# Kernel optimization log

Measured on AMD Instinct MI355X. Metric: run time of the kernel, lower is better.

Reference implementation:

```python
import jax, jax.numpy as jnp
import numpy as np

B, S, D, H, BS, L, FF, V = 2, 4096, 1024, 16, 64, 4, 4096, 50000
HD = D // H; NB = S // BS; NM = NB - 2; R = 3

def layernorm(x, g, b):
    mu = x.mean(-1, keepdims=True)
    var = ((x - mu) ** 2).mean(-1, keepdims=True)
    return (x - mu) * jax.lax.rsqrt(var + 1e-5) * g + b

def bigbird_attn(x, neg, rand_attn, Wq, bq, Wk, bk, Wv, bv, Wo, bo):
    heads = lambda t: t.reshape(B, S, H, HD).transpose(0, 2, 1, 3)
    q, k, v = heads(x @ Wq + bq), heads(x @ Wk + bk), heads(x @ Wv + bv)
    scale = np.float32(1.0 / np.sqrt(HD))
    qb = q.reshape(B, H, NB, BS, HD); kb = k.reshape(B, H, NB, BS, HD); vb = v.reshape(B, H, NB, BS, HD)
    negb = neg.reshape(B, NB, BS)
    # global query blocks (first & last) attend densely to all keys
    qg = jnp.concatenate([qb[:, :, 0], qb[:, :, -1]], axis=2)  # [B,H,2*BS,HD]
    sg = jnp.einsum('bhqd,bhkd->bhqk', qg, k) * scale + neg[:, None, None, :]
    ctx_g = jnp.einsum('bhqk,bhkd->bhqd', jax.nn.softmax(sg, -1), v)
    # middle query blocks: sliding window(3) + global(2) + random(R) key blocks
    win_k = jnp.stack([kb[:, :, i:i + NM] for i in range(3)], axis=3)  # [B,H,NM,3,BS,HD]
    win_v = jnp.stack([vb[:, :, i:i + NM] for i in range(3)], axis=3)
    gidx = jnp.array([0, NB - 1])
    g_k = jnp.broadcast_to(kb[:, :, gidx][:, :, None], (B, H, NM, 2, BS, HD))
    g_v = jnp.broadcast_to(vb[:, :, gidx][:, :, None], (B, H, NM, 2, BS, HD))
    hix = jnp.arange(H)[:, None, None]
    r_k = kb[:, hix, rand_attn]  # [B,H,NM,R,BS,HD]
    r_v = vb[:, hix, rand_attn]
    K = 3 + 2 + R
    keys = jnp.concatenate([win_k, g_k, r_k], axis=3).reshape(B, H, NM, K * BS, HD)
    vals = jnp.concatenate([win_v, g_v, r_v], axis=3).reshape(B, H, NM, K * BS, HD)
    win_m = jnp.stack([negb[:, i:i + NM] for i in range(3)], axis=2)  # [B,NM,3,BS]
    g_m = jnp.broadcast_to(negb[:, gidx][:, None], (B, NM, 2, BS))
    m_wg = jnp.concatenate([win_m, g_m], axis=2).reshape(B, 1, NM, 5 * BS)
    r_m = negb[:, rand_attn].reshape(B, H, NM, R * BS)
    m_all = jnp.concatenate([jnp.broadcast_to(m_wg, (B, H, NM, 5 * BS)), r_m], axis=-1)
    sm = jnp.einsum('bhnqd,bhnkd->bhnqk', qb[:, :, 1:-1], keys) * scale + m_all[:, :, :, None, :]
    ctx_m = jnp.einsum('bhnqk,bhnkd->bhnqd', jax.nn.softmax(sm, -1), vals)
    ctx = jnp.concatenate([ctx_g[:, :, None, :BS], ctx_m, ctx_g[:, :, None, BS:]], axis=2)
    out = ctx.reshape(B, H, S, HD).transpose(0, 2, 1, 3).reshape(B, S, D)
    return out @ Wo + bo

def reference(input_ids, attention_mask, rand_attn, emb, Wq, bq, Wk, bk, Wv, bv, Wo, bo, ln1_g, ln1_b, W1, b1, W2, b2, ln2_g, ln2_b, lnf_g, lnf_b, projW, projb):
    x = emb[input_ids]
    neg = (1.0 - attention_mask.astype(jnp.float32)) * (-1e9)
    for l in range(L):  # pre-norm transformer encoder layers
        x = x + bigbird_attn(layernorm(x, ln1_g[l], ln1_b[l]), neg, rand_attn,
                             Wq[l], bq[l], Wk[l], bk[l], Wv[l], bv[l], Wo[l], bo[l])
        h = layernorm(x, ln2_g[l], ln2_b[l])
        x = x + (jax.nn.gelu(h @ W1[l] + b1[l]) @ W2[l] + b2[l])
    x = layernorm(x, lnf_g, lnf_b)
    feats = x.mean(axis=1)  # pooled output (mean over tokens)
    feats = feats / jnp.maximum(jnp.linalg.norm(feats, axis=-1, keepdims=True), 1e-12)
    return feats @ projW + projb

def setup_inputs():
    key = jax.random.key(0)
    ks = jax.random.split(key, 16)
    init = lambda k, shp: (0.02 * jax.random.normal(k, shp)).astype(jnp.float32)
    return {
        'input_ids': jax.random.randint(ks[0], (B, S), 0, V),
        'attention_mask': jnp.ones((B, S), dtype=jnp.int32),
        'rand_attn': jax.random.randint(ks[1], (H, NM, R), 1, NB - 1),
        'emb': init(ks[2], (V, D)),
        'Wq': init(ks[3], (L, D, D)), 'bq': jnp.zeros((L, D), jnp.float32),
        'Wk': init(ks[4], (L, D, D)), 'bk': jnp.zeros((L, D), jnp.float32),
        'Wv': init(ks[5], (L, D, D)), 'bv': jnp.zeros((L, D), jnp.float32),
        'Wo': init(ks[6], (L, D, D)), 'bo': jnp.zeros((L, D), jnp.float32),
        'ln1_g': jnp.ones((L, D), jnp.float32), 'ln1_b': jnp.zeros((L, D), jnp.float32),
        'W1': init(ks[7], (L, D, FF)), 'b1': jnp.zeros((L, FF), jnp.float32),
        'W2': init(ks[8], (L, FF, D)), 'b2': jnp.zeros((L, D), jnp.float32),
        'ln2_g': jnp.ones((L, D), jnp.float32), 'ln2_b': jnp.zeros((L, D), jnp.float32),
        'lnf_g': jnp.ones((D,), jnp.float32), 'lnf_b': jnp.zeros((D,), jnp.float32),
        'projW': init(ks[9], (D, 512)), 'projb': jnp.zeros((512,), jnp.float32),
    }
```

## Files before the change

### kernel.cpp

```cpp
#include <hip/hip_runtime.h>
#include <hip/hip_bf16.h>
#include <cstdint>
#include <cstddef>

#define BATCH 2
#define SEQ   4096
#define DIM   1024
#define NHEAD 16
#define HDIM  64
#define NBLK  64
#define NMID  62
#define NRAND 3
#define NLAYER 4
#define FFDIM 4096
#define ROWS  (BATCH*SEQ)
#define KSPL  8
#define QKVLD (3*DIM)

using f32x4 = __attribute__((ext_vector_type(4))) float;
using s16x8 = __attribute__((ext_vector_type(8))) short;
using s16x4 = __attribute__((ext_vector_type(4))) short;

__device__ inline float bf2f(short s) {
    unsigned u = ((unsigned)(unsigned short)s) << 16;
    union { unsigned u; float f; } cv; cv.u = u; return cv.f;
}
__device__ inline short f2bf(float f) {
    union { float f; unsigned u; } cv; cv.f = f;
    unsigned u = cv.u;
    unsigned r = (u + 0x7fffu + ((u >> 16) & 1u)) >> 16;
    return (short)r;
}
__device__ inline float gelu_f(float x) {
    float u = 0.7978845608028654f * (x + 0.044715f * x * x * x);
    float a = fabsf(u);
    float th = 1.f - 2.f / (1.f + __expf(2.f * a));
    th = copysignf(th, u);
    return 0.5f * x * (1.f + th);
}

__device__ inline void gload16(const short* g, short* l) {
    __builtin_amdgcn_global_load_lds(
        (const __attribute__((address_space(1))) void*)g,
        (__attribute__((address_space(3))) void*)l,
        16, 0, 0);
}

__global__ __launch_bounds__(256) void embed_kernel(
    const int* __restrict__ ids, const float* __restrict__ emb, float* __restrict__ x)
{
    int row = blockIdx.x;
    int id  = ids[row];
    ((float4*)x)[(size_t)row * 256 + threadIdx.x] =
        ((const float4*)emb)[(size_t)id * 256 + threadIdx.x];
}

__global__ __launch_bounds__(256) void neg_kernel(
    const int* __restrict__ mask, float* __restrict__ neg)
{
    int i = blockIdx.x * 256 + threadIdx.x;
    if (i < ROWS) neg[i] = (1.f - (float)mask[i]) * -1e9f;
}

__global__ __launch_bounds__(256) void biaspack_kernel(
    const float* __restrict__ bq, const float* __restrict__ bk,
    const float* __restrict__ bv, float* __restrict__ b3)
{
    int i = blockIdx.x * 256 + threadIdx.x;
    float v = (i < DIM) ? bq[i] : (i < 2 * DIM) ? bk[i - DIM] : bv[i - 2 * DIM];
    b3[i] = v;
}

template<int OUTBF>
__global__ __launch_bounds__(256) void ln_kernel(
    const float* __restrict__ x, const float* __restrict__ g,
    const float* __restrict__ bia, void* __restrict__ out)
{
    __shared__ float s1[4], s2[4];
    int row = blockIdx.x, t = threadIdx.x;
    const float* xr = x + (size_t)row * DIM;
    float4 v = ((const float4*)xr)[t];
    float s = v.x + v.y + v.z + v.w;
    #pragma unroll
    for (int o = 32; o > 0; o >>= 1) s += __shfl_xor(s, o, 64);
    if ((t & 63) == 0) s1[t >> 6] = s;
    __syncthreads();
    float mu = (s1[0] + s1[1] + s1[2] + s1[3]) * (1.f / DIM);
    float dx = v.x - mu, dy = v.y - mu, dz = v.z - mu, dw = v.w - mu;
    float q = dx*dx + dy*dy + dz*dz + dw*dw;
    #pragma unroll
    for (int o = 32; o > 0; o >>= 1) q += __shfl_xor(q, o, 64);
    if ((t & 63) == 0) s2[t >> 6] = q;
    __syncthreads();
    float var = (s2[0] + s2[1] + s2[2] + s2[3]) * (1.f / DIM);
    float rs  = rsqrtf(var + 1e-5f);
    float4 gg = ((const float4*)g)[t];
    float4 bb = ((const float4*)bia)[t];
    float o0 = dx * rs * gg.x + bb.x;
    float o1 = dy * rs * gg.y + bb.y;
    float o2 = dz * rs * gg.z + bb.z;
    float o3 = dw * rs * gg.w + bb.w;
    if (OUTBF) {
        s16x4 ov = { f2bf(o0), f2bf(o1), f2bf(o2), f2bf(o3) };
        ((s16x4*)out)[(size_t)row * (DIM/4) + t] = ov;
    } else {
        float4 ov = { o0, o1, o2, o3 };
        ((float4*)out)[(size_t)row * (DIM/4) + t] = ov;
    }
}

__global__ __launch_bounds__(256) void wconv_kernel(
    const float* __restrict__ W, short* __restrict__ Wt, int K, int N)
{
    __shared__ float tile[32][33];
    int k0 = blockIdx.x * 32, n0 = blockIdx.y * 32;
    int t = threadIdx.x;
    int r = t >> 3, c = (t & 7) * 4;
    float4 v = *(const float4*)(W + (size_t)(k0 + r) * N + n0 + c);
    tile[r][c+0] = v.x; tile[r][c+1] = v.y; tile[r][c+2] = v.z; tile[r][c+3] = v.w;
    __syncthreads();
    s16x4 ov;
    #pragma unroll
    for (int jj = 0; jj < 4; ++jj) ov[jj] = f2bf(tile[c + jj][r]);
    *(s16x4*)(Wt + (size_t)(n0 + r) * K + k0 + c) = ov;
}

__global__ __launch_bounds__(256) void vtrans_kernel(
    const short* __restrict__ qkv, short* __restrict__ vT)
{
    __shared__ short tile[64][66];
    const int sb = blockIdx.x, h = blockIdx.y, b = blockIdx.z;
    const int t = threadIdx.x;
    {
        int row = t >> 2, c0 = (t & 3) * 16;
        const short* src = qkv + 2 * DIM + (size_t)(b * SEQ + sb * 64 + row) * QKVLD + h * HDIM + c0;
        s16x8 a0 = ((const s16x8*)src)[0];
        s16x8 a1 = ((const s16x8*)src)[1];
        #pragma unroll
        for (int i = 0; i < 8; ++i) { tile[row][c0 + i] = a0[i]; tile[row][c0 + 8 + i] = a1[i]; }
    }
    __syncthreads();
    {
        int d = t >> 2, k0 = (t & 3) * 16;
        s16x8 o0, o1;
        #pragma unroll
        for (int i = 0; i < 8; ++i) { o0[i] = tile[k0 + i][d]; o1[i] = tile[k0 + 8 + i][d]; }
        short* dst = vT + (size_t)((b * NHEAD + h) * HDIM + d) * SEQ + sb * 64 + k0;
        ((s16x8*)dst)[0] = o0;
        ((s16x8*)dst)[1] = o1;
    }
}

template<int EPI>
__global__ __launch_bounds__(512) void gemm256_kernel(
    const short* __restrict__ A, const short* __restrict__ Bt,
    const float* __restrict__ bias, const float* __restrict__ resid,
    void* __restrict__ Cout, int M, int N, int K, int klen)
{
    __shared__ short As[2][256 * 64];
    __shared__ short Bs[2][256 * 64];
    const int t = threadIdx.x;
    const int m0 = blockIdx.x * 256, n0 = blockIdx.y * 256;
    const int lane = t & 63, wave = t >> 6;
    const int wm = wave >> 2, wn = wave & 3;
    const int lrow = lane >> 3;
    const int lksw = ((lane & 7) ^ lrow) * 8;

    f32x4 acc[8][4];
    #pragma unroll
    for (int m = 0; m < 8; ++m)
        #pragma unroll
        for (int n = 0; n < 4; ++n)
            acc[m][n] = f32x4{0.f, 0.f, 0.f, 0.f};

    auto STAGE = [&](int side, int kt) {
        #pragma unroll
        for (int c = 0; c < 4; ++c) {
            int chunk = wave + c * 8;
            int row = chunk * 8 + lrow;
            gload16(A  + (size_t)(m0 + row) * K + kt + lksw, &As[side][chunk * 512]);
            gload16(Bt + (size_t)(n0 + row) * K + kt + lksw, &Bs[side][chunk * 512]);
        }
    };

    const int k0 = blockIdx.z * klen;
    STAGE(0, k0);
    __syncthreads();

    int cur = 0;
    for (int kt = k0; kt < k0 + klen; kt += 64) {
        if (kt + 64 < k0 + klen) STAGE(cur ^ 1, kt + 64);
        const short* Ac = As[cur];
        const short* Bc = Bs[cur];
        #pragma unroll
        for (int kk = 0; kk < 2; ++kk) {
            const int cb = kk * 64 + (lane >> 4) * 16;
            s16x8 bfr[4];
            #pragma unroll
            for (int n = 0; n < 4; ++n) {
                int rB = wn * 64 + n * 16 + (lane & 15);
                bfr[n] = *(const s16x8*)((const char*)Bc + rB * 128 + (cb ^ ((rB & 7) << 4)));
            }
            #pragma unroll
            for (int mq = 0; mq < 4; ++mq) {
                s16x8 af[2];
                #pragma unroll
                for (int i = 0; i < 2; ++i) {
                    int rA = wm * 128 + mq * 32 + i * 16 + (lane & 15);
                    af[i] = *(const s16x8*)((const char*)Ac + rA * 128 + (cb ^ ((rA & 7) << 4)));
                }
                #pragma unroll
                for (int i = 0; i < 2; ++i)
                    #pragma unroll
                    for (int n = 0; n < 4; ++n)
                        acc[mq * 2 + i][n] = __builtin_amdgcn_mfma_f32_16x16x32_bf16(
                            af[i], bfr[n], acc[mq * 2 + i][n], 0, 0, 0);
            }
        }
        __syncthreads();
        cur ^= 1;
    }

    const int rbase = m0 + wm * 128 + ((lane >> 4) << 2);
    const int cbase = n0 + wn * 64 + (lane & 15);
    #pragma unroll
    for (int m = 0; m < 8; ++m) {
        #pragma unroll
        for (int n = 0; n < 4; ++n) {
            #pragma unroll
            for (int j = 0; j < 4; ++j) {
                int row = rbase + m * 16 + j;
                int col = cbase + n * 16;
                size_t idx = (size_t)row * N + col;
                float val = acc[m][n][j];
                if (EPI == 3) {
                    ((float*)Cout)[(size_t)blockIdx.z * ((size_t)M * N) + idx] = val;
                } else {
                    val += bias[col];
                    if (EPI == 1) val = gelu_f(val);
                    ((short*)Cout)[idx] = f2bf(val);
                }
            }
        }
    }
    (void)resid;
}

template<int EPI>
__global__ __launch_bounds__(256) void gemm_kernel(
    const short* __restrict__ A, const short* __restrict__ Bt,
    const float* __restrict__ bias, const float* __restrict__ resid,
    void* __restrict__ Cout, int M, int N, int K, int klen)
{
    __shared__ short As[128 * 64];
    __shared__ short Bs[128 * 64];
    const int t = threadIdx.x;
    const int m0 = blockIdx.x * 128, n0 = blockIdx.y * 128;
    const int lane = t & 63, wave = t >> 6;
    const int wr = (wave >> 1) * 64, wc = (wave & 1) * 64;
    const int lrow = lane >> 3;
    const int lksw = ((lane & 7) ^ lrow) * 8;

    f32x4 acc[4][4];
    #pragma unroll
    for (int m = 0; m < 4; ++m)
        #pragma unroll
        for (int n = 0; n < 4; ++n)
            acc[m][n] = f32x4{0.f, 0.f, 0.f, 0.f};

    const int k0 = blockIdx.z * klen;
    for (int kt = k0; kt < k0 + klen; kt += 64) {
        #pragma unroll
        for (int c = 0; c < 4; ++c) {
            int chunk = wave * 4 + c;
            int row = chunk * 8 + lrow;
            gload16(A  + (size_t)(m0 + row) * K + kt + lksw, As + chunk * 512);
            gload16(Bt + (size_t)(n0 + row) * K + kt + lksw, Bs + chunk * 512);
        }
        asm volatile("s_waitcnt vmcnt(0)" ::: "memory");
        __syncthreads();
        #pragma unroll
        for (int kk = 0; kk < 2; ++kk) {
            s16x8 af[4], bfr[4];
            int cb = kk * 64 + (lane >> 4) * 16;
            #pragma unroll
            for (int i = 0; i < 4; ++i) {
                int rA = wr + i * 16 + (lane & 15);
                af[i]  = *(const s16x8*)((const char*)As + rA * 128 + (cb ^ ((rA & 7) << 4)));
                int rB = wc + i * 16 + (lane & 15);
                bfr[i] = *(const s16x8*)((const char*)Bs + rB * 128 + (cb ^ ((rB & 7) << 4)));
            }
            #pragma unroll
            for (int m = 0; m < 4; ++m)
                #pragma unroll
                for (int n = 0; n < 4; ++n)
                    acc[m][n] = __builtin_amdgcn_mfma_f32_16x16x32_bf16(
                        af[m], bfr[n], acc[m][n], 0, 0, 0);
        }
        __syncthreads();
    }

    const int rbase = m0 + wr + ((lane >> 4) << 2);
    const int cbase = n0 + wc + (lane & 15);
    #pragma unroll
    for (int m = 0; m < 4; ++m) {
        #pragma unroll
        for (int n = 0; n < 4; ++n) {
            #pragma unroll
            for (int j = 0; j < 4; ++j) {
                int row = rbase + m * 16 + j;
                int col = cbase + n * 16;
                size_t idx = (size_t)row * N + col;
                float val = acc[m][n][j] + bias[col];
                if (EPI == 1) val = gelu_f(val);
                if (EPI == 2) ((float*)Cout)[idx] = val + resid[idx];
                else          ((short*)Cout)[idx] = f2bf(val);
            }
        }
    }
}

__global__ __launch_bounds__(256) void kred_kernel(
    const float* __restrict__ part, const float* __restrict__ bias, float* __restrict__ x)
{
    const size_t MN = (size_t)ROWS * DIM;
    size_t idx = (size_t)blockIdx.x * DIM + threadIdx.x * 4;
    float4 p0 = *(const float4*)(part + idx);
    float4 p1 = *(const float4*)(part + MN + idx);
    float4 bb = *(const float4*)(bias + threadIdx.x * 4);
    float4 xv = *(const float4*)(x + idx);
    float4 o = { xv.x + p0.x + p1.x + bb.x,
                 xv.y + p0.y + p1.y + bb.y,
                 xv.z + p0.z + p1.z + bb.z,
                 xv.w + p0.w + p1.w + bb.w };
    *(float4*)(x + idx) = o;
}

__device__ inline void attn_tile_mfma(
    const short* __restrict__ kglob, const short* __restrict__ vtglob,
    const float* __restrict__ negp, int kld,
    short* Ks, short* Vs, float* kmask,
    const s16x8* qfrag, f32x4* o, float& mr, float& lsum)
{
    const int t = threadIdx.x;
    const int lane = t & 63;
    const int q15 = lane & 15, g = lane >> 4;
    const int sw = (lane & 7) << 4;

    {
        int row = t >> 2, c0 = (t & 3) * 16;
        int rsw = (row & 7) << 4;
        const short* ksrc = kglob + (size_t)row * kld + c0;
        s16x8 a0 = ((const s16x8*)ksrc)[0];
        s16x8 a1 = ((const s16x8*)ksrc)[1];
        char* kdst = (char*)Ks + row * 128;
        *(s16x8*)(kdst + ((c0 * 2)      ^ rsw)) = a0;
        *(s16x8*)(kdst + ((c0 * 2 + 16) ^ rsw)) = a1;
        const short* vsrc = vtglob + (size_t)row * SEQ + c0;
        s16x8 b0 = ((const s16x8*)vsrc)[0];
        s16x8 b1 = ((const s16x8*)vsrc)[1];
        char* vdst = (char*)Vs + row * 128;
        *(s16x8*)(vdst + ((c0 * 2)      ^ rsw)) = b0;
        *(s16x8*)(vdst + ((c0 * 2 + 16) ^ rsw)) = b1;
        if (t < 16) ((float4*)kmask)[t] = ((const float4*)negp)[t];
    }
    __syncthreads();

    f32x4 s[4];
    #pragma unroll
    for (int f = 0; f < 4; ++f) s[f] = f32x4{0.f, 0.f, 0.f, 0.f};
    #pragma unroll
    for (int ch = 0; ch < 2; ++ch) {
        #pragma unroll
        for (int f = 0; f < 4; ++f) {
            s16x8 kf = *(const s16x8*)((const char*)Ks + (16 * f + q15) * 128 + ((ch * 64 + g * 16) ^ sw));
            s[f] = __builtin_amdgcn_mfma_f32_16x16x32_bf16(kf, qfrag[ch], s[f], 0, 0, 0);
        }
    }

    float p[4][4];
    float mt = -1e30f;
    #pragma unroll
    for (int f = 0; f < 4; ++f) {
        float4 km = ((const float4*)kmask)[f * 4 + g];
        #pragma unroll
        for (int j = 0; j < 4; ++j) {
            float val = s[f][j] * 0.125f + ((const float*)&km)[j];
            p[f][j] = val;
            mt = fmaxf(mt, val);
        }
    }
    mt = fmaxf(mt, __shfl_xor(mt, 16, 64));
    mt = fmaxf(mt, __shfl_xor(mt, 32, 64));
    float mn = fmaxf(mr, mt);
    float psum = 0.f;
    #pragma unroll
    for (int f = 0; f < 4; ++f)
        #pragma unroll
        for (int j = 0; j < 4; ++j) {
            float e = __expf(p[f][j] - mn);
            p[f][j] = e;
            psum += e;
        }
    psum += __shfl_xor(psum, 16, 64);
    psum += __shfl_xor(psum, 32, 64);
    float fc = __expf(mr - mn);
    mr = mn;
    lsum = lsum * fc + psum;
    #pragma unroll
    for (int dt = 0; dt < 4; ++dt)
        #pragma unroll
        for (int j = 0; j < 4; ++j) o[dt][j] *= fc;

    unsigned pk[4][2];
    #pragma unroll
    for (int f = 0; f < 4; ++f)
        #pragma unroll
        for (int pp = 0; pp < 2; ++pp)
            pk[f][pp] = ((unsigned)(unsigned short)f2bf(p[f][2 * pp + 1]) << 16)
                      |  (unsigned)(unsigned short)f2bf(p[f][2 * pp]);

    const int bsel = (lane >> 4) & 1, asel = (lane >> 5) & 1;
    #pragma unroll
    for (int c = 0; c < 2; ++c) {
        union { s16x8 v; int u[4]; } pb;
        #pragma unroll
        for (int w = 0; w < 4; ++w) {
            int src = q15 + 16 * (2 * bsel + (w >> 1));
            int lo = __shfl((int)pk[2 * c][w & 1], src, 64);
            int hi = __shfl((int)pk[2 * c + 1][w & 1], src, 64);
            pb.u[w] = asel ? hi : lo;
        }
        #pragma unroll
        for (int dt = 0; dt < 4; ++dt) {
            s16x8 vf = *(const s16x8*)((const char*)Vs + (16 * dt + q15) * 128 + ((c * 64 + g * 16) ^ sw));
            o[dt] = __builtin_amdgcn_mfma_f32_16x16x32_bf16(vf, pb.v, o[dt], 0, 0, 0);
        }
    }
    __syncthreads();
}

__device__ inline void stage_q64_swz(const short* __restrict__ qglob, int qld, short* Qs)
{
    int t = threadIdx.x;
    int row = t >> 2, c0 = (t & 3) * 16;
    int rsw = (row & 7) << 4;
    const short* src = qglob + (size_t)row * qld + c0;
    s16x8 a0 = ((const s16x8*)src)[0];
    s16x8 a1 = ((const s16x8*)src)[1];
    char* dst = (char*)Qs + row * 128;
    *(s16x8*)(dst + ((c0 * 2)      ^ rsw)) = a0;
    *(s16x8*)(dst + ((c0 * 2 + 16) ^ rsw)) = a1;
}

__global__ __launch_bounds__(256) void attn_middle_mfma(
    const short* __restrict__ qkv, const short* __restrict__ vT,
    const float* __restrict__ neg, const int* __restrict__ rand_attn, short* __restrict__ ctx)
{
    __shared__ short Qs[64 * 64];
    __shared__ short Ks[64 * 64];
    __shared__ short Vs[64 * 64];
    __shared__ float kmask[64];

    const int j = blockIdx.x, h = blockIdx.y, b = blockIdx.z;
    const int n = j + 1;
    const int t = threadIdx.x;
    const int lane = t & 63, wave = t >> 6;
    const int q15 = lane & 15, g = lane >> 4;
    const int sw = (lane & 7) << 4;

    stage_q64_swz(qkv + (size_t)(b * SEQ + n * 64) * QKVLD + h * HDIM, QKVLD, Qs);
    __syncthreads();

    s16x8 qfrag[2];
    {
        int qrow = wave * 16 + q15;
        #pragma unroll
        for (int ch = 0; ch < 2; ++ch)
            qfrag[ch] = *(const s16x8*)((const char*)Qs + qrow * 128 + ((ch * 64 + g * 16) ^ sw));
    }

    int kbl[8];
    kbl[0] = n - 1; kbl[1] = n; kbl[2] = n + 1; kbl[3] = 0; kbl[4] = NBLK - 1;
    {
        const int* ra = rand_attn + ((size_t)h * NMID + j) * NRAND;
        kbl[5] = ra[0]; kbl[6] = ra[1]; kbl[7] = ra[2];
    }

    f32x4 o[4];
    #pragma unroll
    for (int dt = 0; dt < 4; ++dt) o[dt] = f32x4{0.f, 0.f, 0.f, 0.f};
    float mr = -1e30f, lsum = 0.f;

    const short* kbase  = qkv + DIM + (size_t)b * SEQ * QKVLD + h * HDIM;
    const short* vtbase = vT + (size_t)(b * NHEAD + h) * HDIM * SEQ;
    const float* negb   = neg + (size_t)b * SEQ;

    #pragma unroll 1
    for (int ib = 0; ib < 8; ++ib) {
        int kbn = kbl[ib];
        attn_tile_mfma(kbase + (size_t)kbn * 64 * QKVLD, vtbase + kbn * 64,
                       negb + kbn * 64, QKVLD, Ks, Vs, kmask, qfrag, o, mr, lsum);
    }

    float inv = 1.f / lsum;
    short* obase = ctx + (size_t)(b * SEQ + n * 64 + wave * 16 + q15) * DIM + h * HDIM;
    #pragma unroll
    for (int dt = 0; dt < 4; ++dt) {
        s16x4 ov;
        #pragma unroll
        for (int jj = 0; jj < 4; ++jj) ov[jj] = f2bf(o[dt][jj] * inv);
        *(s16x4*)(obase + dt * 16 + g * 4) = ov;
    }
}

__global__ __launch_bounds__(256) void attn_global_mfma(
    const short* __restrict__ qkv, const short* __restrict__ vT,
    const float* __restrict__ neg, float* __restrict__ part)
{
    __shared__ short Qs[64 * 64];
    __shared__ short Ks[64 * 64];
    __shared__ short Vs[64 * 64];
    __shared__ float kmask[64];

    const int qb = blockIdx.x >> 3, ks = blockIdx.x & 7;
    const int h = blockIdx.y, b = blockIdx.z;
    const int tok0 = qb ? (SEQ - 64) : 0;
    const int t = threadIdx.x;
    const int lane = t & 63, wave = t >> 6;
    const int q15 = lane & 15, g = lane >> 4;
    const int sw = (lane & 7) << 4;

    stage_q64_swz(qkv + (size_t)(b * SEQ + tok0) * QKVLD + h * HDIM, QKVLD, Qs);
    __syncthreads();

    s16x8 qfrag[2];
    {
        int qrow = wave * 16 + q15;
        #pragma unroll
        for (int ch = 0; ch < 2; ++ch)
            qfrag[ch] = *(const s16x8*)((const char*)Qs + qrow * 128 + ((ch * 64 + g * 16) ^ sw));
    }

    f32x4 o[4];
    #pragma unroll
    for (int dt = 0; dt < 4; ++dt) o[dt] = f32x4{0.f, 0.f, 0.f, 0.f};
    float mr = -1e30f, lsum = 0.f;

    const short* kbase  = qkv + DIM + (size_t)b * SEQ * QKVLD + h * HDIM;
    const short* vtbase = vT + (size_t)(b * NHEAD + h) * HDIM * SEQ;
    const float* negb   = neg + (size_t)b * SEQ;

    #pragma unroll 1
    for (int ib = 0; ib < 8; ++ib) {
        int kbn = ks * 8 + ib;
        attn_tile_mfma(kbase + (size_t)kbn * 64 * QKVLD, vtbase + kbn * 64,
                       negb + kbn * 64, QKVLD, Ks, Vs, kmask, qfrag, o, mr, lsum);
    }

    float* pbase = part + ((size_t)(((b * NHEAD + h) * 2 + qb) * KSPL + ks)) * 4224;
    int qrow = wave * 16 + q15;
    #pragma unroll
    for (int dt = 0; dt < 4; ++dt)
        *(f32x4*)(pbase + qrow * 64 + dt * 16 + g * 4) = o[dt];
    if (g == 0) { pbase[4096 + qrow] = mr; pbase[4160 + qrow] = lsum; }
}

__global__ __launch_bounds__(256) void attn_greduce(
    const float* __restrict__ part, short* __restrict__ ctx)
{
    const int qb = blockIdx.x, h = blockIdx.y, b = blockIdx.z;
    const int tok0 = qb ? (SEQ - 64) : 0;
    const int t = threadIdx.x;
    const int qq = t >> 2, d0 = (t & 3) * 16;
    const float* base = part + ((size_t)(((b * NHEAD + h) * 2 + qb) * KSPL)) * 4224;

    float m = -1e30f;
    #pragma unroll 1
    for (int s = 0; s < KSPL; ++s)
        m = fmaxf(m, base[(size_t)s * 4224 + 4096 + qq]);
    float L = 0.f;
    float acc[16];
    #pragma unroll
    for (int i = 0; i < 16; ++i) acc[i] = 0.f;
    #pragma unroll 1
    for (int s = 0; s < KSPL; ++s) {
        const float* bp = base + (size_t)s * 4224;
        float w = __expf(bp[4096 + qq] - m);
        L += w * bp[4160 + qq];
        const float4* row = (const float4*)(bp + qq * 64 + d0);
        #pragma unroll
        for (int v4 = 0; v4 < 4; ++v4) {
            float4 val = row[v4];
            acc[v4 * 4 + 0] = fmaf(w, val.x, acc[v4 * 4 + 0]);
            acc[v4 * 4 + 1] = fmaf(w, val.y, acc[v4 * 4 + 1]);
            acc[v4 * 4 + 2] = fmaf(w, val.z, acc[v4 * 4 + 2]);
            acc[v4 * 4 + 3] = fmaf(w, val.w, acc[v4 * 4 + 3]);
        }
    }
    float inv = 1.f / L;
    short* dst = ctx + (size_t)(b * SEQ + tok0 + qq) * DIM + h * HDIM + d0;
    s16x8 o0, o1;
    #pragma unroll
    for (int i = 0; i < 8; ++i) { o0[i] = f2bf(acc[i] * inv); o1[i] = f2bf(acc[8 + i] * inv); }
    ((s16x8*)dst)[0] = o0;
    ((s16x8*)dst)[1] = o1;
}

__global__ __launch_bounds__(256) void colsum1_kernel(
    const float* __restrict__ xln, float* __restrict__ partial)
{
    const int ch = blockIdx.x, b = blockIdx.y, t = threadIdx.x;
    const float* base = xln + ((size_t)b * SEQ + ch * 32) * DIM + t * 4;
    float4 acc = {0.f, 0.f, 0.f, 0.f};
    #pragma unroll 4
    for (int r = 0; r < 32; ++r) {
        float4 v = *(const float4*)(base + (size_t)r * DIM);
        acc.x += v.x; acc.y += v.y; acc.z += v.z; acc.w += v.w;
    }
    *(float4*)(partial + ((size_t)(b * 128 + ch)) * DIM + t * 4) = acc;
}

__global__ __launch_bounds__(256) void colsum2_kernel(
    const float* __restrict__ partial, float* __restrict__ feats)
{
    const int b = blockIdx.x, t = threadIdx.x;
    float4 acc = {0.f, 0.f, 0.f, 0.f};
    #pragma unroll 1
    for (int ch = 0; ch < 128; ++ch) {
        float4 v = *(const float4*)(partial + ((size_t)(b * 128 + ch)) * DIM + t * 4);
        acc.x += v.x; acc.y += v.y; acc.z += v.z; acc.w += v.w;
    }
    const float is = 1.f / SEQ;
    float4 o = { acc.x * is, acc.y * is, acc.z * is, acc.w * is };
    *(float4*)(feats + (size_t)b * DIM + t * 4) = o;
}

__global__ __launch_bounds__(256) void head_kernel(
    const float* __restrict__ feats, const float* __restrict__ projW,
    const float* __restrict__ projb, float* __restrict__ out)
{
    __shared__ float f[DIM];
    __shared__ float slots[4];
    int b = blockIdx.x, t = threadIdx.x;
    float ss = 0.f;
    for (int i = t; i < DIM; i += 256) {
        float vv = feats[b * DIM + i];
        f[i] = vv;
        ss += vv * vv;
    }
    #pragma unroll
    for (int o = 32; o > 0; o >>= 1) ss += __shfl_xor(ss, o, 64);
    if ((t & 63) == 0) slots[t >> 6] = ss;
    __syncthreads();
    float nrm = sqrtf(slots[0] + slots[1] + slots[2] + slots[3]);
    float inv = 1.f / fmaxf(nrm, 1e-12f);
    for (int o = t; o < 512; o += 256) {
        float acc = 0.f;
        for (int d = 0; d < DIM; ++d)
            acc = fmaf(f[d], projW[(size_t)d * 512 + o], acc);
        out[b * 512 + o] = acc * inv + projb[o];
    }
}

extern "C" void kernel_launch(void* const* d_in, const int* in_sizes, int n_in,
                              void* d_out, int out_size, void* d_ws, size_t ws_size,
                              hipStream_t stream)
{
    (void)in_sizes; (void)n_in; (void)out_size; (void)ws_size;
    const int*   ids   = (const int*)d_in[0];
    const int*   amask = (const int*)d_in[1];
    const int*   rnd   = (const int*)d_in[2];
    const float* emb   = (const float*)d_in[3];
    const float* Wq    = (const float*)d_in[4];
    const float* bq    = (const float*)d_in[5];
    const float* Wk    = (const float*)d_in[6];
    const float* bk    = (const float*)d_in[7];
    const float* Wv    = (const float*)d_in[8];
    const float* bv    = (const float*)d_in[9];
    const float* Wo    = (const float*)d_in[10];
    const float* bo    = (const float*)d_in[11];
    const float* ln1g  = (const float*)d_in[12];
    const float* ln1b  = (const float*)d_in[13];
    const float* W1    = (const float*)d_in[14];
    const float* b1    = (const float*)d_in[15];
    const float* W2    = (const float*)d_in[16];
    const float* b2    = (const float*)d_in[17];
    const float* ln2g  = (const float*)d_in[18];
    const float* ln2b  = (const float*)d_in[19];
    const float* lnfg  = (const float*)d_in[20];
    const float* lnfb  = (const float*)d_in[21];
    const float* projW = (const float*)d_in[22];
    const float* projb = (const float*)d_in[23];
    float* out = (float*)d_out;

    char* ws = (char*)d_ws;
    size_t off = 0;
    float* x    = (float*)(ws + off); off += (size_t)ROWS * DIM * 4;
    float* xn_f = (float*)(ws + off);
    short* xn_b = (short*)(ws + off); off += (size_t)ROWS * DIM * 4;
    short* qkv  = (short*)(ws + off); off += (size_t)ROWS * QKVLD * 2;
    short* vT   = (short*)(ws + off); off += (size_t)ROWS * DIM * 2;
    short* ctxb = (short*)(ws + off); off += (size_t)ROWS * DIM * 2;
    short* ffb  = (short*)(ws + off); off += (size_t)ROWS * FFDIM * 2;
    short* wt   = (short*)(ws + off); off += (size_t)FFDIM * DIM * 2;
    float* neg  = (float*)(ws + off); off += (size_t)ROWS * 4;
    float* bias3= (float*)(ws + off); off += (size_t)QKVLD * 4;
    float* feats= (float*)(ws + off); off += (size_t)BATCH * DIM * 4;
    float* part = (float*)(ws + off); off += (size_t)BATCH * NHEAD * 2 * KSPL * 4224 * 4;
    float* cpart= (float*)(ws + off); off += (size_t)BATCH * 128 * DIM * 4;
    float* ff2p = (float*)qkv;

    embed_kernel<<<ROWS, 256, 0, stream>>>(ids, emb, x);
    neg_kernel<<<(ROWS + 255) / 256, 256, 0, stream>>>(amask, neg);

    for (int l = 0; l < NLAYER; ++l) {
        ln_kernel<1><<<ROWS, 256, 0, stream>>>(x, ln1g + l * DIM, ln1b + l * DIM, xn_b);

        wconv_kernel<<<dim3(DIM/32, DIM/32), 256, 0, stream>>>(Wq + (size_t)l*DIM*DIM, wt,               DIM, DIM);
        wconv_kernel<<<dim3(DIM/32, DIM/32), 256, 0, stream>>>(Wk + (size_t)l*DIM*DIM, wt + 1024*1024,   DIM, DIM);
        wconv_kernel<<<dim3(DIM/32, DIM/32), 256, 0, stream>>>(Wv + (size_t)l*DIM*DIM, wt + 2*1024*1024, DIM, DIM);
        biaspack_kernel<<<QKVLD/256, 256, 0, stream>>>(bq + l*DIM, bk + l*DIM, bv + l*DIM, bias3);
        gemm256_kernel<0><<<dim3(ROWS/256, QKVLD/256), 512, 0, stream>>>(xn_b, wt, bias3, nullptr, qkv, ROWS, QKVLD, DIM, DIM);

        vtrans_kernel<<<dim3(SEQ/64, NHEAD, BATCH), 256, 0, stream>>>(qkv, vT);

        attn_global_mfma<<<dim3(2 * KSPL, NHEAD, BATCH), 256, 0, stream>>>(qkv, vT, neg, part);
        attn_middle_mfma<<<dim3(NMID, NHEAD, BATCH), 256, 0, stream>>>(qkv, vT, neg, rnd, ctxb);
        attn_greduce<<<dim3(2, NHEAD, BATCH), 256, 0, stream>>>(part, ctxb);

        wconv_kernel<<<dim3(DIM/32, DIM/32), 256, 0, stream>>>(Wo + (size_t)l*DIM*DIM, wt, DIM, DIM);
        gemm_kernel<2><<<dim3(ROWS/128, DIM/128), 256, 0, stream>>>(ctxb, wt, bo + l*DIM, x, x, ROWS, DIM, DIM, DIM);

        ln_kernel<1><<<ROWS, 256, 0, stream>>>(x, ln2g + l * DIM, ln2b + l * DIM, xn_b);

        wconv_kernel<<<dim3(DIM/32, FFDIM/32), 256, 0, stream>>>(W1 + (size_t)l*DIM*FFDIM, wt, DIM, FFDIM);
        gemm256_kernel<1><<<dim3(ROWS/256, FFDIM/256), 512, 0, stream>>>(xn_b, wt, b1 + l*FFDIM, nullptr, ffb, ROWS, FFDIM, DIM, DIM);
        wconv_kernel<<<dim3(FFDIM/32, DIM/32), 256, 0, stream>>>(W2 + (size_t)l*FFDIM*DIM, wt, FFDIM, DIM);
        gemm256_kernel<3><<<dim3(ROWS/256, DIM/256, 2), 512, 0, stream>>>(ffb, wt, nullptr, nullptr, ff2p, ROWS, DIM, FFDIM, FFDIM/2);
        kred_kernel<<<ROWS, 256, 0, stream>>>(ff2p, b2 + l*DIM, x);
    }

    ln_kernel<0><<<ROWS, 256, 0, stream>>>(x, lnfg, lnfb, xn_f);
    colsum1_kernel<<<dim3(SEQ/32, BATCH), 256, 0, stream>>>(xn_f, cpart);
    colsum2_kernel<<<BATCH, 256, 0, stream>>>(cpart, feats);
    head_kernel<<<BATCH, 256, 0, stream>>>(feats, projW, projb, out);
}
```

Before: 1.774 ms.

## Batch weight conversion upfront, triple-buffer GEMM with 256x128 tiles, fuse residual-reduce with LayerNorm

All layers' weights are converted to transposed bf16 in a few batched launches before the layer loop, replacing the many per-layer small conversion kernels. The 256-wide GEMM now uses 256x128 tiles with three LDS stages, explicit vmcnt waits, raw barriers and setprio, to overlap global loads with MFMA work and add more workgroups. The split-K reduction kernel is fused with the following LayerNorm, which drops a separate LN pass over the activations per layer. The cost is a larger workspace holding all layers' converted weights, and hand-written waitcnt logic that depends on the exact count of loads issued per stage.

New measurement: 2.196 ms. 23.8% more time.

```diff
diff --git a/kernel.cpp b/kernel.cpp
--- a/kernel.cpp
+++ b/kernel.cpp
@@ -16,6 +16,7 @@
 #define ROWS  (BATCH*SEQ)
 #define KSPL  8
 #define QKVLD (3*DIM)
+#define WLAYER (12*1024*1024)
 
 using f32x4 = __attribute__((ext_vector_type(4))) float;
 using s16x8 = __attribute__((ext_vector_type(8))) short;
@@ -67,8 +68,11 @@
     const float* __restrict__ bv, float* __restrict__ b3)
 {
     int i = blockIdx.x * 256 + threadIdx.x;
-    float v = (i < DIM) ? bq[i] : (i < 2 * DIM) ? bk[i - DIM] : bv[i - 2 * DIM];
-    b3[i] = v;
+    int l = blockIdx.y;
+    float v = (i < DIM) ? bq[l * DIM + i]
+            : (i < 2 * DIM) ? bk[l * DIM + i - DIM]
+            : bv[l * DIM + i - 2 * DIM];
+    b3[(size_t)l * QKVLD + i] = v;
 }
 
 template<int OUTBF>
@@ -109,8 +113,8 @@
     }
 }
 
-__global__ __launch_bounds__(256) void wconv_kernel(
-    const float* __restrict__ W, short* __restrict__ Wt, int K, int N)
+__device__ inline void wconv_body(const float* __restrict__ W, short* __restrict__ Wt,
+                                  int K, int N)
 {
     __shared__ float tile[32][33];
     int k0 = blockIdx.x * 32, n0 = blockIdx.y * 32;
@@ -123,6 +127,25 @@
     #pragma unroll
     for (int jj = 0; jj < 4; ++jj) ov[jj] = f2bf(tile[c + jj][r]);
     *(s16x4*)(Wt + (size_t)(n0 + r) * K + k0 + c) = ov;
+}
+
+__global__ __launch_bounds__(256) void wconv4_kernel(
+    const float* __restrict__ Wq, const float* __restrict__ Wk,
+    const float* __restrict__ Wv, const float* __restrict__ Wo,
+    short* __restrict__ wt4)
+{
+    int z = blockIdx.z, l = z >> 2, m = z & 3;
+    const float* W = (m == 0 ? Wq : m == 1 ? Wk : m == 2 ? Wv : Wo) + (size_t)l * DIM * DIM;
+    short* Wt = wt4 + (size_t)l * WLAYER + (size_t)m * 1024 * 1024;
+    wconv_body(W, Wt, DIM, DIM);
+}
+
+__global__ __launch_bounds__(256) void wconvff_kernel(
+    const float* __restrict__ W, short* __restrict__ wt4,
+    int K, int N, size_t dstOff)
+{
+    int l = blockIdx.z;
+    wconv_body(W + (size_t)l * DIM * FFDIM, wt4 + (size_t)l * WLAYER + dstOff, K, N);
 }
 
 __global__ __launch_bounds__(256) void vtrans_kernel(
@@ -154,79 +177,100 @@
 template<int EPI>
 __global__ __launch_bounds__(512) void gemm256_kernel(
     const short* __restrict__ A, const short* __restrict__ Bt,
-    const float* __restrict__ bias, const float* __restrict__ resid,
-    void* __restrict__ Cout, int M, int N, int K, int klen)
-{
-    __shared__ short As[2][256 * 64];
-    __shared__ short Bs[2][256 * 64];
+    const float* __restrict__ bias, void* __restrict__ Cout,
+    int M, int N, int K, int klen)
+{
+    __shared__ short As[3][256 * 64];
+    __shared__ short Bs[3][128 * 64];
     const int t = threadIdx.x;
-    const int m0 = blockIdx.x * 256, n0 = blockIdx.y * 256;
+    const int m0 = blockIdx.x * 256, n0 = blockIdx.y * 128;
     const int lane = t & 63, wave = t >> 6;
     const int wm = wave >> 2, wn = wave & 3;
+    const int l15 = lane & 15;
     const int lrow = lane >> 3;
     const int lksw = ((lane & 7) ^ lrow) * 8;
 
-    f32x4 acc[8][4];
+    f32x4 acc[8][2];
     #pragma unroll
     for (int m = 0; m < 8; ++m)
         #pragma unroll
-        for (int n = 0; n < 4; ++n)
+        for (int n = 0; n < 2; ++n)
             acc[m][n] = f32x4{0.f, 0.f, 0.f, 0.f};
 
     auto STAGE = [&](int side, int kt) {
         #pragma unroll
         for (int c = 0; c < 4; ++c) {
-            int chunk = wave + c * 8;
-            int row = chunk * 8 + lrow;
-            gload16(A  + (size_t)(m0 + row) * K + kt + lksw, &As[side][chunk * 512]);
-            gload16(Bt + (size_t)(n0 + row) * K + kt + lksw, &Bs[side][chunk * 512]);
+            int chunk = wave * 4 + c;
+            gload16(A + (size_t)(m0 + chunk * 8 + lrow) * K + kt + lksw,
+                    &As[side][chunk * 512]);
+        }
+        #pragma unroll
+        for (int c = 0; c < 2; ++c) {
+            int chunk = wave * 2 + c;
+            gload16(Bt + (size_t)(n0 + chunk * 8 + lrow) * K + kt + lksw,
+                    &Bs[side][chunk * 512]);
         }
     };
 
     const int k0 = blockIdx.z * klen;
+    const int T = klen >> 6;
     STAGE(0, k0);
-    __syncthreads();
-
-    int cur = 0;
-    for (int kt = k0; kt < k0 + klen; kt += 64) {
-        if (kt + 64 < k0 + klen) STAGE(cur ^ 1, kt + 64);
-        const short* Ac = As[cur];
-        const short* Bc = Bs[cur];
-        #pragma unroll
-        for (int kk = 0; kk < 2; ++kk) {
-            const int cb = kk * 64 + (lane >> 4) * 16;
-            s16x8 bfr[4];
+    if (T > 1) {
+        STAGE(1, k0 + 64);
+        asm volatile("s_waitcnt vmcnt(6)" ::: "memory");
+    } else {
+        asm volatile("s_waitcnt vmcnt(0)" ::: "memory");
+    }
+    __builtin_amdgcn_s_barrier();
+
+    for (int ti = 0; ti < T; ++ti) {
+        const int side = ti % 3;
+        if (ti + 2 < T) STAGE((ti + 2) % 3, k0 + (ti + 2) * 64);
+
+        const short* Ac = As[side];
+        const short* Bc = Bs[side];
+        s16x8 bfr[2][2];
+        #pragma unroll
+        for (int nf = 0; nf < 2; ++nf)
             #pragma unroll
-            for (int n = 0; n < 4; ++n) {
-                int rB = wn * 64 + n * 16 + (lane & 15);
-                bfr[n] = *(const s16x8*)((const char*)Bc + rB * 128 + (cb ^ ((rB & 7) << 4)));
+            for (int kk = 0; kk < 2; ++kk) {
+                int r = wn * 32 + nf * 16 + l15;
+                int cb = kk * 64 + (lane >> 4) * 16;
+                bfr[nf][kk] = *(const s16x8*)((const char*)Bc + r * 128 + (cb ^ ((r & 7) << 4)));
+            }
+        __builtin_amdgcn_s_setprio(1);
+        #pragma unroll
+        for (int mf = 0; mf < 8; ++mf) {
+            s16x8 af[2];
+            #pragma unroll
+            for (int kk = 0; kk < 2; ++kk) {
+                int r = wm * 128 + mf * 16 + l15;
+                int cb = kk * 64 + (lane >> 4) * 16;
+                af[kk] = *(const s16x8*)((const char*)Ac + r * 128 + (cb ^ ((r & 7) << 4)));
             }
             #pragma unroll
-            for (int mq = 0; mq < 4; ++mq) {
-                s16x8 af[2];
+            for (int kk = 0; kk < 2; ++kk)
                 #pragma unroll
-                for (int i = 0; i < 2; ++i) {
-                    int rA = wm * 128 + mq * 32 + i * 16 + (lane & 15);
-                    af[i] = *(const s16x8*)((const char*)Ac + rA * 128 + (cb ^ ((rA & 7) << 4)));
-                }
-                #pragma unroll
-                for (int i = 0; i < 2; ++i)
-                    #pragma unroll
-                    for (int n = 0; n < 4; ++n)
-                        acc[mq * 2 + i][n] = __builtin_amdgcn_mfma_f32_16x16x32_bf16(
-                            af[i], bfr[n], acc[mq * 2 + i][n], 0, 0, 0);
-            }
-        }
-        __syncthreads();
-        cur ^= 1;
+                for (int nf = 0; nf < 2; ++nf)
+                    acc[mf][nf] = __builtin_amdgcn_mfma_f32_16x16x32_bf16(
+                        af[kk], bfr[nf][kk], acc[mf][nf], 0, 0, 0);
+        }
+        __builtin_amdgcn_s_setprio(0);
+        __builtin_amdgcn_sched_barrier(0);
+        if (ti + 2 < T) {
+            asm volatile("s_waitcnt vmcnt(6)" ::: "memory");
+        } else if (ti + 1 < T) {
+            asm volatile("s_waitcnt vmcnt(0)" ::: "memory");
+        }
+        __builtin_amdgcn_s_barrier();
     }
 
     const int rbase = m0 + wm * 128 + ((lane >> 4) << 2);
-    const int cbase = n0 + wn * 64 + (lane & 15);
+    const int cbase = n0 + wn * 32 + l15;
     #pragma unroll
     for (int m = 0; m < 8; ++m) {
         #pragma unroll
-        for (int n = 0; n < 4; ++n) {
+        for (int n = 0; n < 2; ++n) {
             #pragma unroll
             for (int j = 0; j < 4; ++j) {
                 int row = rbase + m * 16 + j;
@@ -243,7 +287,6 @@
             }
         }
     }
-    (void)resid;
 }
 
 template<int EPI>
@@ -320,20 +363,53 @@
     }
 }
 
-__global__ __launch_bounds__(256) void kred_kernel(
-    const float* __restrict__ part, const float* __restrict__ bias, float* __restrict__ x)
-{
+template<int MODE>
+__global__ __launch_bounds__(256) void kred_ln_kernel(
+    const float* __restrict__ part, const float* __restrict__ bias,
+    const float* __restrict__ g, const float* __restrict__ bvec,
+    float* __restrict__ x, void* __restrict__ xn)
+{
+    __shared__ float s1[4], s2[4];
     const size_t MN = (size_t)ROWS * DIM;
-    size_t idx = (size_t)blockIdx.x * DIM + threadIdx.x * 4;
+    const int row = blockIdx.x, t = threadIdx.x;
+    size_t idx = (size_t)row * DIM + t * 4;
     float4 p0 = *(const float4*)(part + idx);
     float4 p1 = *(const float4*)(part + MN + idx);
-    float4 bb = *(const float4*)(bias + threadIdx.x * 4);
+    float4 bb = *(const float4*)(bias + t * 4);
     float4 xv = *(const float4*)(x + idx);
-    float4 o = { xv.x + p0.x + p1.x + bb.x,
+    float4 v = { xv.x + p0.x + p1.x + bb.x,
                  xv.y + p0.y + p1.y + bb.y,
                  xv.z + p0.z + p1.z + bb.z,
                  xv.w + p0.w + p1.w + bb.w };
-    *(float4*)(x + idx) = o;
+    if (MODE == 0) *(float4*)(x + idx) = v;
+
+    float s = v.x + v.y + v.z + v.w;
+    #pragma unroll
+    for (int o = 32; o > 0; o >>= 1) s += __shfl_xor(s, o, 64);
+    if ((t & 63) == 0) s1[t >> 6] = s;
+    __syncthreads();
+    float mu = (s1[0] + s1[1] + s1[2] + s1[3]) * (1.f / DIM);
+    float dx = v.x - mu, dy = v.y - mu, dz = v.z - mu, dw = v.w - mu;
+    float q = dx*dx + dy*dy + dz*dz + dw*dw;
+    #pragma unroll
+    for (int o = 32; o > 0; o >>= 1) q += __shfl_xor(q, o, 64);
+    if ((t & 63) == 0) s2[t >> 6] = q;
+    __syncthreads();
+    float var = (s2[0] + s2[1] + s2[2] + s2[3]) * (1.f / DIM);
+    float rs  = rsqrtf(var + 1e-5f);
+    float4 gg = ((const float4*)g)[t];
+    float4 b2 = ((const float4*)bvec)[t];
+    float o0 = dx * rs * gg.x + b2.x;
+    float o1 = dy * rs * gg.y + b2.y;
+    float o2 = dz * rs * gg.z + b2.z;
+    float o3 = dw * rs * gg.w + b2.w;
+    if (MODE == 0) {
+        s16x4 ov = { f2bf(o0), f2bf(o1), f2bf(o2), f2bf(o3) };
+        ((s16x4*)xn)[(size_t)row * (DIM/4) + t] = ov;
+    } else {
+        float4 ov = { o0, o1, o2, o3 };
+        ((float4*)xn)[(size_t)row * (DIM/4) + t] = ov;
+    }
 }
 
 __device__ inline void attn_tile_mfma(
@@ -703,9 +779,9 @@
     short* vT   = (short*)(ws + off); off += (size_t)ROWS * DIM * 2;
     short* ctxb = (short*)(ws + off); off += (size_t)ROWS * DIM * 2;
     short* ffb  = (short*)(ws + off); off += (size_t)ROWS * FFDIM * 2;
-    short* wt   = (short*)(ws + off); off += (size_t)FFDIM * DIM * 2;
+    short* wt4  = (short*)(ws + off); off += (size_t)NLAYER * WLAYER * 2;
     float* neg  = (float*)(ws + off); off += (size_t)ROWS * 4;
-    float* bias3= (float*)(ws + off); off += (size_t)QKVLD * 4;
+    float* bias3= (float*)(ws + off); off += (size_t)NLAYER * QKVLD * 4;
     float* feats= (float*)(ws + off); off += (size_t)BATCH * DIM * 4;
     float* part = (float*)(ws + off); off += (size_t)BATCH * NHEAD * 2 * KSPL * 4224 * 4;
     float* cpart= (float*)(ws + off); off += (size_t)BATCH * 128 * DIM * 4;
@@ -714,14 +790,21 @@
     embed_kernel<<<ROWS, 256, 0, stream>>>(ids, emb, x);
     neg_kernel<<<(ROWS + 255) / 256, 256, 0, stream>>>(amask, neg);
 
+    wconv4_kernel<<<dim3(DIM/32, DIM/32, NLAYER*4), 256, 0, stream>>>(Wq, Wk, Wv, Wo, wt4);
+    wconvff_kernel<<<dim3(DIM/32, FFDIM/32, NLAYER), 256, 0, stream>>>(W1, wt4, DIM, FFDIM, (size_t)4*1024*1024);
+    wconvff_kernel<<<dim3(FFDIM/32, DIM/32, NLAYER), 256, 0, stream>>>(W2, wt4, FFDIM, DIM, (size_t)8*1024*1024);
+    biaspack_kernel<<<dim3(QKVLD/256, NLAYER), 256, 0, stream>>>(bq, bk, bv, bias3);
+
     for (int l = 0; l < NLAYER; ++l) {
-        ln_kernel<1><<<ROWS, 256, 0, stream>>>(x, ln1g + l * DIM, ln1b + l * DIM, xn_b);
-
-        wconv_kernel<<<dim3(DIM/32, DIM/32), 256, 0, stream>>>(Wq + (size_t)l*DIM*DIM, wt,               DIM, DIM);
-        wconv_kernel<<<dim3(DIM/32, DIM/32), 256, 0, stream>>>(Wk + (size_t)l*DIM*DIM, wt + 1024*1024,   DIM, DIM);
-        wconv_kernel<<<dim3(DIM/32, DIM/32), 256, 0, stream>>>(Wv + (size_t)l*DIM*DIM, wt + 2*1024*1024, DIM, DIM);
-        biaspack_kernel<<<QKVLD/256, 256, 0, stream>>>(bq + l*DIM, bk + l*DIM, bv + l*DIM, bias3);
-        gemm256_kernel<0><<<dim3(ROWS/256, QKVLD/256), 512, 0, stream>>>(xn_b, wt, bias3, nullptr, qkv, ROWS, QKVLD, DIM, DIM);
+        short* wq3 = wt4 + (size_t)l * WLAYER;
+        short* wo  = wq3 + 3 * 1024 * 1024;
+        short* w1t = wo  + 1024 * 1024;
+        short* w2t = w1t + 4 * 1024 * 1024;
+
+        if (l == 0)
+            ln_kernel<1><<<ROWS, 256, 0, stream>>>(x, ln1g, ln1b, xn_b);
+
+        gemm256_kernel<0><<<dim3(ROWS/256, QKVLD/128), 512, 0, stream>>>(xn_b, wq3, bias3 + (size_t)l*QKVLD, qkv, ROWS, QKVLD, DIM, DIM);
 
         vtrans_kernel<<<dim3(SEQ/64, NHEAD, BATCH), 256, 0, stream>>>(qkv, vT);
 
@@ -729,19 +812,19 @@
         attn_middle_mfma<<<dim3(NMID, NHEAD, BATCH), 256, 0, stream>>>(qkv, vT, neg, rnd, ctxb);
         attn_greduce<<<dim3(2, NHEAD, BATCH), 256, 0, stream>>>(part, ctxb);
 
-        wconv_kernel<<<dim3(DIM/32, DIM/32), 256, 0, stream>>>(Wo + (size_t)l*DIM*DIM, wt, DIM, DIM);
-        gemm_kernel<2><<<dim3(ROWS/128, DIM/128), 256, 0, stream>>>(ctxb, wt, bo + l*DIM, x, x, ROWS, DIM, DIM, DIM);
+        gemm_kernel<2><<<dim3(ROWS/128, DIM/128), 256, 0, stream>>>(ctxb, wo, bo + l*DIM, x, x, ROWS, DIM, DIM, DIM);
 
         ln_kernel<1><<<ROWS, 256, 0, stream>>>(x, ln2g + l * DIM, ln2b + l * DIM, xn_b);
 
-        wconv_kernel<<<dim3(DIM/32, FFDIM/32), 256, 0, stream>>>(W1 + (size_t)l*DIM*FFDIM, wt, DIM, FFDIM);
-        gemm256_kernel<1><<<dim3(ROWS/256, FFDIM/256), 512, 0, stream>>>(xn_b, wt, b1 + l*FFDIM, nullptr, ffb, ROWS, FFDIM, DIM, DIM);
-        wconv_kernel<<<dim3(FFDIM/32, DIM/32), 256, 0, stream>>>(W2 + (size_t)l*FFDIM*DIM, wt, FFDIM, DIM);
-        gemm256_kernel<3><<<dim3(ROWS/256, DIM/256, 2), 512, 0, stream>>>(ffb, wt, nullptr, nullptr, ff2p, ROWS, DIM, FFDIM, FFDIM/2);
-        kred_kernel<<<ROWS, 256, 0, stream>>>(ff2p, b2 + l*DIM, x);
-    }
-
-    ln_kernel<0><<<ROWS, 256, 0, stream>>>(x, lnfg, lnfb, xn_f);
+        gemm256_kernel<1><<<dim3(ROWS/256, FFDIM/128), 512, 0, stream>>>(xn_b, w1t, b1 + l*FFDIM, ffb, ROWS, FFDIM, DIM, DIM);
+        gemm256_kernel<3><<<dim3(ROWS/256, DIM/128, 2), 512, 0, stream>>>(ffb, w2t, nullptr, ff2p, ROWS, DIM, FFDIM, FFDIM/2);
+
+        if (l < NLAYER - 1)
+            kred_ln_kernel<0><<<ROWS, 256, 0, stream>>>(ff2p, b2 + l*DIM, ln1g + (l+1)*DIM, ln1b + (l+1)*DIM, x, xn_b);
+        else
+            kred_ln_kernel<1><<<ROWS, 256, 0, stream>>>(ff2p, b2 + l*DIM, lnfg, lnfb, x, xn_f);
+    }
+
     colsum1_kernel<<<dim3(SEQ/32, BATCH), 256, 0, stream>>>(xn_f, cpart);
     colsum2_kernel<<<BATCH, 256, 0, stream>>>(cpart, feats);
     head_kernel<<<BATCH, 256, 0, stream>>>(feats, projW, projb, out);
```
